# Performance work log

Hardware: AMD Instinct MI355X
Metric: run time of the kernel (lower is better)

Reference implementation:

```python
import jax, jax.numpy as jnp
import numpy as np
import math

B, T, C, H = 2, 2048, 1024, 16
HD = C // H
WINDOW = 256  # local_attn_ctx with attnblocksize=1


def setup_inputs() -> dict:
    key = jax.random.key(0)
    k1, k2, k3 = jax.random.split(key, 3)
    x = jax.random.normal(k1, (B, T, C), dtype=jnp.float32)
    Wqkv = jax.random.normal(k2, (C, 3 * C), dtype=jnp.float32) * 0.02
    bqkv = jnp.zeros((3 * C,), dtype=jnp.float32)
    Wproj = jax.random.normal(k3, (C, C), dtype=jnp.float32) * 0.02
    bproj = jnp.zeros((C,), dtype=jnp.float32)
    # 'local' block-sparse layout at token granularity: causal + sliding window
    i = np.arange(T)[:, None]
    j = np.arange(T)[None, :]
    mask = ((j <= i) & (i - j <= WINDOW)).astype(np.int32)
    return {"x": x, "Wqkv": Wqkv, "bqkv": bqkv, "Wproj": Wproj, "bproj": bproj,
            "mask": jnp.asarray(mask)}


def reference(x, Wqkv, bqkv, Wproj, bproj, mask):
    Bb, Tt, Cc = x.shape
    qkv = (x @ Wqkv + bqkv).reshape(Bb, Tt, 3, H, HD)  # [B,T,3,H,hd]
    q = jnp.transpose(qkv[:, :, 0], (0, 2, 1, 3))  # [B,H,T,hd]
    k = jnp.transpose(qkv[:, :, 1], (0, 2, 1, 3))
    v = jnp.transpose(qkv[:, :, 2], (0, 2, 1, 3))
    scale = 1.0 / math.sqrt(HD)
    att = jnp.einsum('bhqd,bhkd->bhqk', q, k) * scale  # dense T x T scores
    att = jnp.where(mask[:Tt, :Tt] == 0, -jnp.inf, att)
    att = jax.nn.softmax(att, axis=-1)
    y = jnp.einsum('bhqk,bhkd->bhqd', att, v)
    y = jnp.transpose(y, (0, 2, 1, 3)).reshape(Bb, Tt, Cc)
    return y @ Wproj + bproj
```

## Files before the change

### kernel.cpp

```cpp
#include <hip/hip_runtime.h>
#include <hip/hip_bf16.h>
#include <math.h>

typedef __bf16 bf16;
typedef __attribute__((ext_vector_type(8))) __bf16 bf16x8;
typedef __attribute__((ext_vector_type(4))) __bf16 bf16x4;
typedef __attribute__((ext_vector_type(4))) float f32x4;

#define B_  2
#define T_  2048
#define C_  1024
#define H_  16
#define HD_ 64
#define WIN_ 256

#define GLOAD16(g, l)                                                        \
  __builtin_amdgcn_global_load_lds(                                          \
      (const __attribute__((address_space(1))) void*)(g),                    \
      (__attribute__((address_space(3))) void*)(l), 16, 0, 0)


__global__ __launch_bounds__(256) void cvt_f32_bf16_k(const float* __restrict__ in,
                                                      bf16* __restrict__ out) {
  int idx = blockIdx.x * 256 + threadIdx.x;
  const float4 v = ((const float4*)in)[idx];
  bf16x4 o;
  o[0] = (bf16)v.x; o[1] = (bf16)v.y; o[2] = (bf16)v.z; o[3] = (bf16)v.w;
  ((bf16x4*)out)[idx] = o;
}

__global__ __launch_bounds__(256) void transpose_cvt_k(const float* __restrict__ W,
                                                       bf16* __restrict__ WT,
                                                       int K, int N) {
  __shared__ float t[32][33];
  int n0 = blockIdx.x * 32, k0 = blockIdx.y * 32;
  int tx = threadIdx.x, ty = threadIdx.y;
  #pragma unroll
  for (int i = 0; i < 32; i += 8)
    t[ty + i][tx] = W[(size_t)(k0 + ty + i) * N + (n0 + tx)];
  __syncthreads();
  #pragma unroll
  for (int i = 0; i < 32; i += 8)
    WT[(size_t)(n0 + ty + i) * K + (k0 + tx)] = (bf16)t[tx][ty + i];
}


template <int BM, int MODE>
__global__ __launch_bounds__(256) void gemm_lds_k(const bf16* __restrict__ A,
                                                  const bf16* __restrict__ Bt,
                                                  const float* __restrict__ bias,
                                                  void* __restrict__ out0,
                                                  void* __restrict__ out1,
                                                  int M, int N, int K) {
  constexpr int FM = BM / 32;
  const int bm = blockIdx.x * BM;
  const int bn = blockIdx.y * 128;
  const int tid  = threadIdx.x;
  const int wid  = tid >> 6;
  const int lane = tid & 63;
  const int wm = (wid >> 1) * (BM / 2);
  const int wn = (wid & 1) * 64;
  const int lr = lane & 15;
  const int g  = lane >> 4;

  __shared__ bf16 As[BM][32];
  __shared__ bf16 Bs[128][32];

  f32x4 acc[FM][4] = {};

  const int srow = lane >> 2;
  const int scol = (lane & 3) * 8;
  const bf16* Abase = A  + (size_t)bm * K;
  const bf16* Bbase = Bt + (size_t)bn * K;

  for (int k0 = 0; k0 < K; k0 += 32) {
    #pragma unroll
    for (int i = 0; i < BM / 64; ++i) {
      const int c = wid * (BM / 64) + i;
      GLOAD16(Abase + (size_t)(c * 16 + srow) * K + k0 + scol, &As[c * 16][0]);
    }
    #pragma unroll
    for (int i = 0; i < 2; ++i) {
      const int c = wid * 2 + i;
      GLOAD16(Bbase + (size_t)(c * 16 + srow) * K + k0 + scol, &Bs[c * 16][0]);
    }
    __syncthreads();

    bf16x8 af[FM], bfr[4];
    #pragma unroll
    for (int m = 0; m < FM; ++m) af[m]  = *(const bf16x8*)&As[wm + m * 16 + lr][g * 8];
    #pragma unroll
    for (int n = 0; n < 4; ++n)  bfr[n] = *(const bf16x8*)&Bs[wn + n * 16 + lr][g * 8];

    #pragma unroll
    for (int m = 0; m < FM; ++m)
      #pragma unroll
      for (int n = 0; n < 4; ++n)
        acc[m][n] = __builtin_amdgcn_mfma_f32_16x16x32_bf16(af[m], bfr[n], acc[m][n], 0, 0, 0);
    __syncthreads();
  }

  const int orow = g * 4;
  const int ocol = lr;
  #pragma unroll
  for (int m = 0; m < FM; ++m)
    #pragma unroll
    for (int n = 0; n < 4; ++n) {
      const int gn  = bn + wn + n * 16 + ocol;
      const int gm0 = bm + wm + m * 16 + orow;
      const float bv = bias[gn];
      if (MODE == 0) {
        #pragma unroll
        for (int r = 0; r < 4; ++r)
          ((float*)out0)[(size_t)(gm0 + r) * N + gn] = acc[m][n][r] + bv;
      } else {
        if (bn < 2 * C_) {
          #pragma unroll
          for (int r = 0; r < 4; ++r)
            ((bf16*)out0)[(size_t)(gm0 + r) * (2 * C_) + gn] = (bf16)(acc[m][n][r] + bv);
        } else {
          const int vcol = gn - 2 * C_;
          const int h = vcol >> 6, d = vcol & 63;
          const int b = gm0 >> 11, tok = gm0 & (T_ - 1);
          bf16x4 o;
          #pragma unroll
          for (int r = 0; r < 4; ++r) o[r] = (bf16)(acc[m][n][r] + bv);
          *(bf16x4*)&((bf16*)out1)[(((size_t)b * H_ + h) * HD_ + d) * T_ + tok] = o;
        }
      }
    }
}


__global__ __launch_bounds__(256) void attn_mfma_k(const bf16* __restrict__ qk,
                                                   const bf16* __restrict__ vt,
                                                   bf16* __restrict__ y) {
  const int q0 = blockIdx.x * 64;
  const int h  = blockIdx.y;
  const int b  = blockIdx.z;
  const int tid  = threadIdx.x;
  const int wid  = tid >> 6;
  const int lane = tid & 63;
  const int lr = lane & 15;
  const int g  = lane >> 4;

  __shared__ bf16 Ks[64][72];
  __shared__ bf16 Vs[64][72];
  __shared__ bf16 Ps[4][16][72];

  const int qrow = q0 + wid * 16 + lr;
  const bf16* qptr = qk + ((size_t)(b * T_ + qrow)) * (2 * C_) + h * HD_;
  bf16x8 qf[2];
  qf[0] = *(const bf16x8*)(qptr + g * 8);
  qf[1] = *(const bf16x8*)(qptr + 32 + g * 8);

  float m = -1e30f, l = 0.f;
  f32x4 yacc[4] = {};

  const int kt_lo = (blockIdx.x >= 4) ? (int)blockIdx.x - 4 : 0;
  for (int kt = kt_lo; kt <= (int)blockIdx.x; ++kt) {
    __syncthreads();
    #pragma unroll
    for (int i = 0; i < 2; ++i) {
      int cc = tid + i * 256;
      int rr = cc >> 3;
      int c0 = (cc & 7) * 8;
      *(bf16x8*)&Ks[rr][c0] = *(const bf16x8*)&qk[((size_t)(b * T_) + kt * 64 + rr) * (2 * C_) + C_ + h * HD_ + c0];
      *(bf16x8*)&Vs[rr][c0] = *(const bf16x8*)&vt[(((size_t)b * H_ + h) * HD_ + rr) * T_ + kt * 64 + c0];
    }
    __syncthreads();

    f32x4 sacc[4] = {};
    #pragma unroll
    for (int t = 0; t < 4; ++t)
      #pragma unroll
      for (int s = 0; s < 2; ++s)
        sacc[t] = __builtin_amdgcn_mfma_f32_16x16x32_bf16(
            *(const bf16x8*)&Ks[t * 16 + lr][s * 32 + g * 8], qf[s], sacc[t], 0, 0, 0);

    float pv[4][4];
    float rmax = -1e30f;
    #pragma unroll
    for (int t = 0; t < 4; ++t)
      #pragma unroll
      for (int r = 0; r < 4; ++r) {
        const int key = kt * 64 + t * 16 + g * 4 + r;
        const bool valid = (key <= qrow) && (qrow - key <= WIN_);
        const float sv = valid ? sacc[t][r] * 0.125f : -__builtin_inff();
        pv[t][r] = sv;
        rmax = fmaxf(rmax, sv);
      }
    rmax = fmaxf(rmax, __shfl_xor(rmax, 16));
    rmax = fmaxf(rmax, __shfl_xor(rmax, 32));

    const float mnew = fmaxf(m, rmax);
    const float alpha = __expf(m - mnew);
    m = mnew;
    float lsum = 0.f;
    #pragma unroll
    for (int t = 0; t < 4; ++t)
      #pragma unroll
      for (int r = 0; r < 4; ++r) {
        const float e = __expf(pv[t][r] - mnew);
        pv[t][r] = e;
        lsum += e;
      }
    lsum += __shfl_xor(lsum, 16);
    lsum += __shfl_xor(lsum, 32);
    l = l * alpha + lsum;

    #pragma unroll
    for (int t = 0; t < 4; ++t) {
      bf16x4 pk;
      #pragma unroll
      for (int r = 0; r < 4; ++r) pk[r] = (bf16)pv[t][r];
      *(bf16x4*)&Ps[wid][lr][t * 16 + g * 4] = pk;
    }

    float al[4];
    #pragma unroll
    for (int r = 0; r < 4; ++r) al[r] = __shfl(alpha, g * 4 + r);
    #pragma unroll
    for (int t = 0; t < 4; ++t)
      #pragma unroll
      for (int r = 0; r < 4; ++r) yacc[t][r] *= al[r];

    bf16x8 pf[2];
    pf[0] = *(const bf16x8*)&Ps[wid][lr][g * 8];
    pf[1] = *(const bf16x8*)&Ps[wid][lr][32 + g * 8];
    #pragma unroll
    for (int t = 0; t < 4; ++t)
      #pragma unroll
      for (int s = 0; s < 2; ++s)
        yacc[t] = __builtin_amdgcn_mfma_f32_16x16x32_bf16(
            pf[s], *(const bf16x8*)&Vs[t * 16 + lr][s * 32 + g * 8], yacc[t], 0, 0, 0);
  }

  float li[4];
  #pragma unroll
  for (int r = 0; r < 4; ++r) li[r] = 1.f / __shfl(l, g * 4 + r);
  #pragma unroll
  for (int t = 0; t < 4; ++t)
    #pragma unroll
    for (int r = 0; r < 4; ++r) {
      const int tok = q0 + wid * 16 + g * 4 + r;
      y[((size_t)(b * T_ + tok)) * C_ + h * HD_ + t * 16 + lr] = (bf16)(yacc[t][r] * li[r]);
    }
}


extern "C" void kernel_launch(void* const* d_in, const int* in_sizes, int n_in,
                              void* d_out, int out_size, void* d_ws, size_t ws_size,
                              hipStream_t stream) {
  const float* x     = (const float*)d_in[0];
  const float* Wqkv  = (const float*)d_in[1];
  const float* bqkv  = (const float*)d_in[2];
  const float* Wproj = (const float*)d_in[3];
  const float* bproj = (const float*)d_in[4];
  float* out = (float*)d_out;

  const size_t SZ_QK  = (size_t)B_ * T_ * 2 * C_ * sizeof(bf16);
  const size_t SZ_VT  = (size_t)B_ * H_ * HD_ * T_ * sizeof(bf16);
  const size_t SZ_XB  = (size_t)B_ * T_ * C_ * sizeof(bf16);
  const size_t SZ_WQT = (size_t)3 * C_ * C_ * sizeof(bf16);
  const size_t SZ_WPT = (size_t)C_ * C_ * sizeof(bf16);
  const size_t NEED   = SZ_QK + SZ_VT + SZ_XB + SZ_WQT + SZ_WPT + SZ_XB;
  if (ws_size < NEED) return;

  char* ws = (char*)d_ws;
  bf16* qkb    = (bf16*)(ws);
  bf16* vtb    = (bf16*)(ws + SZ_QK);
  bf16* xb     = (bf16*)(ws + SZ_QK + SZ_VT);
  bf16* wqkvT  = (bf16*)(ws + SZ_QK + SZ_VT + SZ_XB);
  bf16* wprojT = (bf16*)(ws + SZ_QK + SZ_VT + SZ_XB + SZ_WQT);
  bf16* yb     = (bf16*)(ws + SZ_QK + SZ_VT + SZ_XB + SZ_WQT + SZ_WPT);

  cvt_f32_bf16_k<<<4096, 256, 0, stream>>>(x, xb);
  transpose_cvt_k<<<dim3(3 * C_ / 32, C_ / 32), dim3(32, 8), 0, stream>>>(Wqkv, wqkvT, C_, 3 * C_);
  transpose_cvt_k<<<dim3(C_ / 32, C_ / 32), dim3(32, 8), 0, stream>>>(Wproj, wprojT, C_, C_);

  gemm_lds_k<128, 2><<<dim3((B_ * T_) / 128, (3 * C_) / 128), 256, 0, stream>>>(
      xb, wqkvT, bqkv, qkb, vtb, B_ * T_, 3 * C_, C_);

  attn_mfma_k<<<dim3(T_ / 64, H_, B_), 256, 0, stream>>>(qkb, vtb, yb);

  gemm_lds_k<64, 0><<<dim3((B_ * T_) / 64, C_ / 128), 256, 0, stream>>>(
      yb, wprojT, bproj, out, nullptr, B_ * T_, C_, C_);
}
```

Before: 96.95 us.

## Add 256x256 double-buffered QKV GEMM with swizzled LDS and async global loads

Replaces the QKV projection GEMM with a new kernel that uses 256x256 tiles, 512 threads, and double-buffered LDS. Tiles are filled through direct global-to-LDS loads with an XOR swizzle, and waits are bounded by vmcnt so the next tile's loads overlap the current tile's MFMA work. The aim is more data reuse per tile and hidden load latency. In exchange the kernel needs much more LDS and many accumulator registers, and the grid drops to 16x12 = 192 blocks, which can leave CUs idle.

```diff
diff --git a/kernel.cpp b/kernel.cpp
--- a/kernel.cpp
+++ b/kernel.cpp
@@ -42,6 +42,116 @@
   #pragma unroll
   for (int i = 0; i < 32; i += 8)
     WT[(size_t)(n0 + ty + i) * K + (k0 + tx)] = (bf16)t[tx][ty + i];
+}
+
+
+template <int MODE>
+__global__ __launch_bounds__(512, 2) void gemm256_k(const bf16* __restrict__ A,
+                                                    const bf16* __restrict__ Bt,
+                                                    const float* __restrict__ bias,
+                                                    void* __restrict__ out0,
+                                                    void* __restrict__ out1,
+                                                    int M, int N, int K) {
+  const int bm = blockIdx.x * 256;
+  const int bn = blockIdx.y * 256;
+  const int tid  = threadIdx.x;
+  const int wid  = tid >> 6;
+  const int lane = tid & 63;
+  const int wr = wid >> 2;
+  const int wc = wid & 3;
+  const int lr = lane & 15;
+  const int g  = lane >> 4;
+
+  __shared__ bf16 As[2][256][64];
+  __shared__ bf16 Bs[2][256][64];
+
+  f32x4 acc[8][4] = {};
+
+  const int rloc = lane >> 3;
+  const int scol = ((lane & 7) ^ rloc) << 3;
+  const bf16* A0 = A  + (size_t)(bm + wid * 32 + rloc) * K + scol;
+  const bf16* B0 = Bt + (size_t)(bn + wid * 32 + rloc) * K + scol;
+  bf16* Al[2] = { &As[0][wid * 32][0], &As[1][wid * 32][0] };
+  bf16* Bl[2] = { &Bs[0][wid * 32][0], &Bs[1][wid * 32][0] };
+
+  #define STAGE(buf, kt)                                                     \
+    do {                                                                     \
+      _Pragma("unroll")                                                      \
+      for (int i = 0; i < 4; ++i) {                                          \
+        GLOAD16(A0 + (size_t)(i * 8) * K + ((kt) << 6), Al[buf] + i * 512);  \
+        GLOAD16(B0 + (size_t)(i * 8) * K + ((kt) << 6), Bl[buf] + i * 512);  \
+      }                                                                      \
+    } while (0)
+
+  const int NT = K >> 6;
+  const int arow = wr * 128 + lr;
+  const int brow = wc * 64 + lr;
+  const int sw   = lr & 7;
+
+  STAGE(0, 0);
+
+  for (int kt = 0; kt < NT; ++kt) {
+    if (kt + 1 < NT) {
+      STAGE((kt + 1) & 1, kt + 1);
+      asm volatile("s_waitcnt vmcnt(8)" ::: "memory");
+    } else {
+      asm volatile("s_waitcnt vmcnt(0)" ::: "memory");
+    }
+    __builtin_amdgcn_s_barrier();
+
+    const bf16 (*Ab)[64] = As[kt & 1];
+    const bf16 (*Bb)[64] = Bs[kt & 1];
+    #pragma unroll
+    for (int s = 0; s < 2; ++s) {
+      bf16x8 af[8], bfv[4];
+      #pragma unroll
+      for (int m = 0; m < 8; ++m)
+        af[m] = *(const bf16x8*)&Ab[arow + m * 16][(((s << 2) + g) ^ sw) << 3];
+      #pragma unroll
+      for (int n = 0; n < 4; ++n)
+        bfv[n] = *(const bf16x8*)&Bb[brow + n * 16][(((s << 2) + g) ^ sw) << 3];
+      __builtin_amdgcn_s_setprio(1);
+      #pragma unroll
+      for (int m = 0; m < 8; ++m)
+        #pragma unroll
+        for (int n = 0; n < 4; ++n)
+          acc[m][n] = __builtin_amdgcn_mfma_f32_16x16x32_bf16(af[m], bfv[n], acc[m][n], 0, 0, 0);
+      __builtin_amdgcn_s_setprio(0);
+    }
+    asm volatile("" ::: "memory");
+    __builtin_amdgcn_s_barrier();
+  }
+  #undef STAGE
+
+  const int orow = g * 4;
+  #pragma unroll
+  for (int n = 0; n < 4; ++n) {
+    const int gn = bn + wc * 64 + n * 16 + lr;
+    const float bv = bias[gn];
+    #pragma unroll
+    for (int m = 0; m < 8; ++m) {
+      const int gm0 = bm + wr * 128 + m * 16 + orow;
+      if (MODE == 0) {
+        #pragma unroll
+        for (int r = 0; r < 4; ++r)
+          ((float*)out0)[(size_t)(gm0 + r) * N + gn] = acc[m][n][r] + bv;
+      } else {
+        if (bn + wc * 64 + n * 16 < 2 * C_) {
+          #pragma unroll
+          for (int r = 0; r < 4; ++r)
+            ((bf16*)out0)[(size_t)(gm0 + r) * (2 * C_) + gn] = (bf16)(acc[m][n][r] + bv);
+        } else {
+          const int vcol = gn - 2 * C_;
+          const int h = vcol >> 6, d = vcol & 63;
+          const int b = gm0 >> 11, tok = gm0 & (T_ - 1);
+          bf16x4 o;
+          #pragma unroll
+          for (int r = 0; r < 4; ++r) o[r] = (bf16)(acc[m][n][r] + bv);
+          *(bf16x4*)&((bf16*)out1)[(((size_t)b * H_ + h) * HD_ + d) * T_ + tok] = o;
+        }
+      }
+    }
+  }
 }
 
 
@@ -113,20 +223,6 @@
         #pragma unroll
         for (int r = 0; r < 4; ++r)
           ((float*)out0)[(size_t)(gm0 + r) * N + gn] = acc[m][n][r] + bv;
-      } else {
-        if (bn < 2 * C_) {
-          #pragma unroll
-          for (int r = 0; r < 4; ++r)
-            ((bf16*)out0)[(size_t)(gm0 + r) * (2 * C_) + gn] = (bf16)(acc[m][n][r] + bv);
-        } else {
-          const int vcol = gn - 2 * C_;
-          const int h = vcol >> 6, d = vcol & 63;
-          const int b = gm0 >> 11, tok = gm0 & (T_ - 1);
-          bf16x4 o;
-          #pragma unroll
-          for (int r = 0; r < 4; ++r) o[r] = (bf16)(acc[m][n][r] + bv);
-          *(bf16x4*)&((bf16*)out1)[(((size_t)b * H_ + h) * HD_ + d) * T_ + tok] = o;
-        }
       }
     }
 }
@@ -279,7 +375,7 @@
   transpose_cvt_k<<<dim3(3 * C_ / 32, C_ / 32), dim3(32, 8), 0, stream>>>(Wqkv, wqkvT, C_, 3 * C_);
   transpose_cvt_k<<<dim3(C_ / 32, C_ / 32), dim3(32, 8), 0, stream>>>(Wproj, wprojT, C_, C_);
 
-  gemm_lds_k<128, 2><<<dim3((B_ * T_) / 128, (3 * C_) / 128), 256, 0, stream>>>(
+  gemm256_k<2><<<dim3((B_ * T_) / 256, (3 * C_) / 256), 512, 0, stream>>>(
       xb, wqkvT, bqkv, qkb, vtb, B_ * T_, 3 * C_, C_);
 
   attn_mfma_k<<<dim3(T_ / 64, H_, B_), 256, 0, stream>>>(qkb, vtb, yb);
```

Result: slower. 101.1 us (+4.3%).

## Replace GEMM with multi-buffered, swizzled, deeper-prefetch MFMA kernel and larger tiles

Applied to the files above, without the earlier changes.

Replaces the single-buffered LDS GEMM with a templated kernel that uses a 4-slot LDS ring. It prefetches two k-tiles ahead using vmcnt-based waits and needs only one barrier per iteration. Source columns are XOR-swizzled to cut LDS bank conflicts, and s_setprio is raised around the MFMA block. The QKV projection now uses 256x256 tiles with 8 waves and the output projection uses 128x128 tiles. These larger tiles reduce the QKV grid to 192 blocks, which may underfill the CUs, and the 128KB of LDS per block limits occupancy.

```diff
diff --git a/kernel.cpp b/kernel.cpp
--- a/kernel.cpp
+++ b/kernel.cpp
@@ -45,76 +45,104 @@
 }
 
 
-template <int BM, int MODE>
-__global__ __launch_bounds__(256) void gemm_lds_k(const bf16* __restrict__ A,
-                                                  const bf16* __restrict__ Bt,
-                                                  const float* __restrict__ bias,
-                                                  void* __restrict__ out0,
-                                                  void* __restrict__ out1,
-                                                  int M, int N, int K) {
-  constexpr int FM = BM / 32;
-  const int bm = blockIdx.x * BM;
-  const int bn = blockIdx.y * 128;
+template <int TM, int TN, int WM, int WN, int MODE>
+__global__ __launch_bounds__(WM * WN * 64, 2)
+void gemm_dp_k(const bf16* __restrict__ A, const bf16* __restrict__ Bt,
+               const float* __restrict__ bias,
+               void* __restrict__ out0, void* __restrict__ out1,
+               int M, int N, int K) {
+  constexpr int NW    = WM * WN;
+  constexpr int WROWS = TM / WM;
+  constexpr int WCOLS = TN / WN;
+  constexpr int FM    = WROWS / 16;
+  constexpr int FN    = WCOLS / 16;
+  constexpr int CA    = TM / 16 / NW;
+  constexpr int CB    = TN / 16 / NW;
+
+  const int bm = blockIdx.x * TM;
+  const int bn = blockIdx.y * TN;
   const int tid  = threadIdx.x;
   const int wid  = tid >> 6;
   const int lane = tid & 63;
-  const int wm = (wid >> 1) * (BM / 2);
-  const int wn = (wid & 1) * 64;
+  const int wr = wid / WN;
+  const int wc = wid % WN;
   const int lr = lane & 15;
   const int g  = lane >> 4;
 
-  __shared__ bf16 As[BM][32];
-  __shared__ bf16 Bs[128][32];
-
-  f32x4 acc[FM][4] = {};
-
-  const int srow = lane >> 2;
-  const int scol = (lane & 3) * 8;
-  const bf16* Abase = A  + (size_t)bm * K;
-  const bf16* Bbase = Bt + (size_t)bn * K;
-
-  for (int k0 = 0; k0 < K; k0 += 32) {
-    #pragma unroll
-    for (int i = 0; i < BM / 64; ++i) {
-      const int c = wid * (BM / 64) + i;
-      GLOAD16(Abase + (size_t)(c * 16 + srow) * K + k0 + scol, &As[c * 16][0]);
-    }
-    #pragma unroll
-    for (int i = 0; i < 2; ++i) {
-      const int c = wid * 2 + i;
-      GLOAD16(Bbase + (size_t)(c * 16 + srow) * K + k0 + scol, &Bs[c * 16][0]);
-    }
-    __syncthreads();
-
-    bf16x8 af[FM], bfr[4];
-    #pragma unroll
-    for (int m = 0; m < FM; ++m) af[m]  = *(const bf16x8*)&As[wm + m * 16 + lr][g * 8];
-    #pragma unroll
-    for (int n = 0; n < 4; ++n)  bfr[n] = *(const bf16x8*)&Bs[wn + n * 16 + lr][g * 8];
-
+  __shared__ bf16 As[4][TM][32];
+  __shared__ bf16 Bs[4][TN][32];
+
+  f32x4 acc[FM][FN] = {};
+
+  const int rloc = lane >> 2;
+  const int scol = (((lane & 3) ^ (rloc & 3))) * 8;
+  const bf16* aSrc = A  + (size_t)(bm + wid * CA * 16 + rloc) * K + scol;
+  const bf16* bSrc = Bt + (size_t)(bn + wid * CB * 16 + rloc) * K + scol;
+
+  #define STAGE_DP(buf, kt)                                                   \
+    do {                                                                      \
+      _Pragma("unroll")                                                       \
+      for (int i = 0; i < CA; ++i)                                            \
+        GLOAD16(aSrc + (size_t)(i * 16) * K + (kt) * 32,                      \
+                &As[buf][(wid * CA + i) * 16][0]);                            \
+      _Pragma("unroll")                                                       \
+      for (int i = 0; i < CB; ++i)                                            \
+        GLOAD16(bSrc + (size_t)(i * 16) * K + (kt) * 32,                      \
+                &Bs[buf][(wid * CB + i) * 16][0]);                            \
+    } while (0)
+
+  const int NT = K >> 5;
+  const int kc = (g ^ (lr & 3)) * 8;
+
+  STAGE_DP(0, 0);
+  STAGE_DP(1, 1);
+
+  for (int t = 0; t < NT; ++t) {
+    const int buf = t & 3;
+    if (t + 2 < NT) {
+      STAGE_DP((t + 2) & 3, t + 2);
+      asm volatile("s_waitcnt vmcnt(8)" ::: "memory");
+    } else if (t + 1 < NT) {
+      asm volatile("s_waitcnt vmcnt(4)" ::: "memory");
+    } else {
+      asm volatile("s_waitcnt vmcnt(0)" ::: "memory");
+    }
+    __builtin_amdgcn_s_barrier();
+    asm volatile("" ::: "memory");
+
+    bf16x8 af[FM], bfv[FN];
     #pragma unroll
     for (int m = 0; m < FM; ++m)
-      #pragma unroll
-      for (int n = 0; n < 4; ++n)
-        acc[m][n] = __builtin_amdgcn_mfma_f32_16x16x32_bf16(af[m], bfr[n], acc[m][n], 0, 0, 0);
-    __syncthreads();
+      af[m] = *(const bf16x8*)&As[buf][wr * WROWS + m * 16 + lr][kc];
+    #pragma unroll
+    for (int n = 0; n < FN; ++n)
+      bfv[n] = *(const bf16x8*)&Bs[buf][wc * WCOLS + n * 16 + lr][kc];
+
+    __builtin_amdgcn_s_setprio(1);
+    #pragma unroll
+    for (int m = 0; m < FM; ++m)
+      #pragma unroll
+      for (int n = 0; n < FN; ++n)
+        acc[m][n] = __builtin_amdgcn_mfma_f32_16x16x32_bf16(af[m], bfv[n], acc[m][n], 0, 0, 0);
+    __builtin_amdgcn_s_setprio(0);
   }
+  #undef STAGE_DP
 
   const int orow = g * 4;
-  const int ocol = lr;
-  #pragma unroll
-  for (int m = 0; m < FM; ++m)
-    #pragma unroll
-    for (int n = 0; n < 4; ++n) {
-      const int gn  = bn + wn + n * 16 + ocol;
-      const int gm0 = bm + wm + m * 16 + orow;
-      const float bv = bias[gn];
+  #pragma unroll
+  for (int n = 0; n < FN; ++n) {
+    const int nbase = bn + wc * WCOLS + n * 16;
+    const int gn = nbase + lr;
+    const float bv = bias[gn];
+    #pragma unroll
+    for (int m = 0; m < FM; ++m) {
+      const int gm0 = bm + wr * WROWS + m * 16 + orow;
       if (MODE == 0) {
         #pragma unroll
         for (int r = 0; r < 4; ++r)
           ((float*)out0)[(size_t)(gm0 + r) * N + gn] = acc[m][n][r] + bv;
       } else {
-        if (bn < 2 * C_) {
+        if (nbase < 2 * C_) {
           #pragma unroll
           for (int r = 0; r < 4; ++r)
             ((bf16*)out0)[(size_t)(gm0 + r) * (2 * C_) + gn] = (bf16)(acc[m][n][r] + bv);
@@ -129,6 +157,7 @@
         }
       }
     }
+  }
 }
 
 
@@ -279,11 +308,11 @@
   transpose_cvt_k<<<dim3(3 * C_ / 32, C_ / 32), dim3(32, 8), 0, stream>>>(Wqkv, wqkvT, C_, 3 * C_);
   transpose_cvt_k<<<dim3(C_ / 32, C_ / 32), dim3(32, 8), 0, stream>>>(Wproj, wprojT, C_, C_);
 
-  gemm_lds_k<128, 2><<<dim3((B_ * T_) / 128, (3 * C_) / 128), 256, 0, stream>>>(
+  gemm_dp_k<256, 256, 2, 4, 2><<<dim3((B_ * T_) / 256, (3 * C_) / 256), 512, 0, stream>>>(
       xb, wqkvT, bqkv, qkb, vtb, B_ * T_, 3 * C_, C_);
 
   attn_mfma_k<<<dim3(T_ / 64, H_, B_), 256, 0, stream>>>(qkb, vtb, yb);
 
-  gemm_lds_k<64, 0><<<dim3((B_ * T_) / 64, C_ / 128), 256, 0, stream>>>(
+  gemm_dp_k<128, 128, 2, 2, 0><<<dim3((B_ * T_) / 128, C_ / 128), 256, 0, stream>>>(
       yb, wprojT, bproj, out, nullptr, B_ * T_, C_, C_);
 }
```

Measured after the change: 96.77 us. About the same (-0.2%).
